# Performance work log

Measured on AMD Instinct MI355X. Metric: run time of the kernel, lower is better.

Reference implementation:

```python
import jax, jax.numpy as jnp
import numpy as np

# SE(3)-equivariant CNN (e3nn/se3cnn-style). The steerable-kernel basis (Clebsch-
# Gordan angular solutions x radial profiles) is a FIXED, non-learned tensor; its
# generating code was not provided, so we use a deterministic random stand-in
# basis of the same shape/contraction structure: kernel = einsum(weights, basis).

K = 7          # conv kernel size
STRIDE = 2
PAD = 3
EPS = 1e-5
BLOCKS = [
    dict(so=8,  vo=4, si=1,  vi=0),
    dict(so=8,  vo=4, si=8,  vi=4),
    dict(so=16, vo=4, si=8,  vi=4),
    dict(so=64, vo=0, si=16, vi=4),
]

def rs_in(b):
    r = [(b['si'], 1)]
    if b['vi'] > 0:
        r += [(b['vi'], 3), (b['vi'], 9)]   # scalars, vectors, 3x3 tensors
    return r

def rs_out(b):
    r = [(b['so'], 1)]
    if b['vo'] > 0:
        r += [(b['vo'], 3)]
    return r

def n_basis(do, di):
    return 3 * min(do, di)   # 3 radial profiles x angular paths (stand-in count)

def _make_bases():
    bases = {}
    for bi, b in enumerate(BLOCKS):
        for oi, (_, do) in enumerate(rs_out(b)):
            for ii, (_, di) in enumerate(rs_in(b)):
                nb = n_basis(do, di)
                rng = np.random.RandomState(1000 * bi + 10 * oi + ii)
                arr = rng.randn(nb, do, di, K, K, K).astype(np.float32)
                bases[(bi, oi, ii)] = jnp.asarray(arr / np.sqrt(nb * di * K ** 3))
    return bases

BASES = _make_bases()

def assemble_kernel(bi, ws):
    b = BLOCKS[bi]
    rows, k = [], 0
    for oi, (mo, do) in enumerate(rs_out(b)):
        cols = []
        for ii, (mi, di) in enumerate(rs_in(b)):
            basis = BASES[(bi, oi, ii)]  # [nb, do, di, K, K, K]
            blk = jnp.einsum('oin,nabxyz->oaibxyz', ws[k], basis)
            cols.append(blk.reshape(mo * do, mi * di, K, K, K))
            k += 1
        rows.append(jnp.concatenate(cols, axis=1))
    return jnp.concatenate(rows, axis=0)  # [C_out, C_in, K, K, K]

def block_forward(bi, x, ws, g_s, g_v, bias):
    b = BLOCKS[bi]
    si, vi, so, vo = b['si'], b['vi'], b['so'], b['vo']
    if vi > 0:  # TensorProduct: outer product of each vector field with itself
        B, _, D, H, W = x.shape
        v = x[:, si:si + 3 * vi].reshape(B, vi, 3, D, H, W)
        t = jnp.einsum('bvixyz,bvjxyz->bvijxyz', v, v).reshape(B, vi * 9, D, H, W)
        x = jnp.concatenate([x, t], axis=1)
    kern = assemble_kernel(bi, ws)
    y = jax.lax.conv_general_dilated(x, kern, (STRIDE,) * 3, [(PAD, PAD)] * 3,
                                     dimension_numbers=('NCDHW', 'OIDHW', 'NCDHW'))
    # SE3BatchNorm (training stats) + BiasRelu (relu on scalars only)
    s = y[:, :so]
    m = s.mean(axis=(0, 2, 3, 4), keepdims=True)
    var = ((s - m) ** 2).mean(axis=(0, 2, 3, 4), keepdims=True)
    s = (s - m) / jnp.sqrt(var + EPS) * g_s[None, :, None, None, None]
    s = jax.nn.relu(s + bias[None, :, None, None, None])
    if vo > 0:
        B2, _, D2, H2, W2 = y.shape
        v = y[:, so:].reshape(B2, vo, 3, D2, H2, W2)
        n2 = (v ** 2).sum(axis=2).mean(axis=(0, 2, 3, 4))  # [vo] mean field norm^2
        v = v / jnp.sqrt(n2 + EPS)[None, :, None, None, None, None]
        v = v * g_v[None, :, None, None, None, None]
        return jnp.concatenate([s, v.reshape(B2, vo * 3, D2, H2, W2)], axis=1)
    return s

def _forward(x, w0_0, w0_1, w1_0, w1_1, w1_2, w1_3, w1_4, w1_5,
             w2_0, w2_1, w2_2, w2_3, w2_4, w2_5, w3_0, w3_1, w3_2,
             g0_s, g0_v, g1_s, g1_v, g2_s, g2_v, g3_s,
             bias0, bias1, bias2, bias3, bn_g, bn_b, lin_w, lin_b):
    ws = [[w0_0, w0_1], [w1_0, w1_1, w1_2, w1_3, w1_4, w1_5],
          [w2_0, w2_1, w2_2, w2_3, w2_4, w2_5], [w3_0, w3_1, w3_2]]
    g_s = [g0_s, g1_s, g2_s, g3_s]
    g_v = [g0_v, g1_v, g2_v, None]
    bias = [bias0, bias1, bias2, bias3]
    # bn_in: BatchNorm3d(1, affine=False), training stats
    m = x.mean(axis=(0, 2, 3, 4), keepdims=True)
    v = ((x - m) ** 2).mean(axis=(0, 2, 3, 4), keepdims=True)
    x = (x - m) / jnp.sqrt(v + EPS)
    for bi in range(4):
        x = block_forward(bi, x, ws[bi], g_s[bi], g_v[bi], bias[bi])
    x = x.mean(axis=(2, 3, 4))  # global spatial mean -> [B, 64]
    mu = x.mean(axis=0, keepdims=True)
    var = ((x - mu) ** 2).mean(axis=0, keepdims=True)
    x = (x - mu) / jnp.sqrt(var + EPS) * bn_g + bn_b
    return x @ lin_w + lin_b

def setup_inputs():
    key = jax.random.key(0)
    ki = [0]
    def nk():
        ki[0] += 1
        return jax.random.fold_in(key, ki[0])
    inp = {'x': jax.random.normal(nk(), (16, 1, 64, 64, 64), dtype=jnp.float32)}
    for bi, b in enumerate(BLOCKS):
        j = 0
        for (mo, do) in rs_out(b):
            for (mi, di) in rs_in(b):
                nb = n_basis(do, di)
                inp[f'w{bi}_{j}'] = 0.2 * jax.random.normal(nk(), (mo, mi, nb), dtype=jnp.float32)
                j += 1
        inp[f'g{bi}_s'] = jnp.ones((b['so'],), jnp.float32)
        if b['vo'] > 0:
            inp[f'g{bi}_v'] = jnp.ones((b['vo'],), jnp.float32)
        inp[f'bias{bi}'] = jnp.zeros((b['so'],), jnp.float32)
    inp['bn_g'] = jnp.ones((64,), jnp.float32)
    inp['bn_b'] = jnp.zeros((64,), jnp.float32)
    inp['lin_w'] = 0.1 * jax.random.normal(nk(), (64, 10), dtype=jnp.float32)
    inp['lin_b'] = jnp.zeros((10,), jnp.float32)
    return inp

def reference(x, w0_0, w0_1, w1_0, w1_1, w1_2, w1_3, w1_4, w1_5,
              w2_0, w2_1, w2_2, w2_3, w2_4, w2_5, w3_0, w3_1, w3_2,
              g0_s, g0_v, g1_s, g1_v, g2_s, g2_v, g3_s,
              bias0, bias1, bias2, bias3, bn_g, bn_b, lin_w, lin_b):
    return _forward(x, w0_0, w0_1, w1_0, w1_1, w1_2, w1_3, w1_4, w1_5,
                    w2_0, w2_1, w2_2, w2_3, w2_4, w2_5, w3_0, w3_1, w3_2,
                    g0_s, g0_v, g1_s, g1_v, g2_s, g2_v, g3_s,
                    bias0, bias1, bias2, bias3, bn_g, bn_b, lin_w, lin_b)
```

## Files before the change

kernel.cpp:

```cpp
#include <hip/hip_runtime.h>
#include <cmath>

constexpr long XN_OFF   = 0;
constexpr long Y0_OFF   = 4194304;
constexpr long Y1_OFF   = 14680064;
constexpr long Y2_OFF   = 15990784;
constexpr long Y3_OFF   = 16220160;
constexpr long K0_OFF   = 16285696;
constexpr long K1_OFF   = 16293536;
constexpr long K2_OFF   = 16732576;
constexpr long K3_OFF   = 17347232;
constexpr long BAS_OFF  = 18952864;
constexpr long SCR_OFF  = 19225552;
constexpr long PARTD_OFF = 20182872;
constexpr long SSD_OFF   = 20191064;
constexpr long ISTD_OFF  = 20191320;
constexpr long POOLD_OFF = 20191324;

struct GenDesc {
  double sdiv[17];
  int seed[17], n[17], scr_off[17], L[17], basis_off[17];
};
struct AsmDesc {
  const float* w[17];
  int cum[18];
  int basis_off[17], row_off[17], col_off[17];
  int dd[17], di[17], mi[17], nb[17], citot[17];
  long koff[17];
};

__global__ __launch_bounds__(256)
void mt_fill_kernel(unsigned int* __restrict__ scratch, GenDesc d) {
  __shared__ unsigned int mt[624];
  const int bb = blockIdx.x;
  const int tid = threadIdx.x;
  if (tid == 0) {
    unsigned int s = (unsigned int)d.seed[bb];
    for (int pos = 0; pos < 624; pos++) {
      mt[pos] = s;
      s = 1812433253u * (s ^ (s >> 30)) + (unsigned)pos + 1u;
    }
  }
  __syncthreads();
  unsigned int* out = scratch + d.scr_off[bb];
  const int L = d.L[bb];
  const int ntw = (L + 623) / 624;
  for (int t = 0; t < ntw; t++) {
    unsigned int v1 = 0, v2 = 0;
    if (tid < 227) { v1 = mt[tid]; v2 = mt[tid + 1]; }
    __syncthreads();
    if (tid < 227) {
      unsigned int y = (v1 & 0x80000000u) | (v2 & 0x7fffffffu);
      mt[tid] = mt[tid + 397] ^ (y >> 1) ^ ((y & 1u) ? 0x9908b0dfu : 0u);
    }
    __syncthreads();
    if (tid < 227) { v1 = mt[227 + tid]; v2 = mt[228 + tid]; }
    __syncthreads();
    if (tid < 227) {
      unsigned int y = (v1 & 0x80000000u) | (v2 & 0x7fffffffu);
      mt[227 + tid] = mt[tid] ^ (y >> 1) ^ ((y & 1u) ? 0x9908b0dfu : 0u);
    }
    __syncthreads();
    if (tid < 170) {
      int i = 454 + tid;
      v1 = mt[i]; v2 = (i < 623) ? mt[i + 1] : mt[0];
    }
    __syncthreads();
    if (tid < 170) {
      int i = 454 + tid;
      unsigned int y = (v1 & 0x80000000u) | (v2 & 0x7fffffffu);
      mt[i] = mt[i - 227] ^ (y >> 1) ^ ((y & 1u) ? 0x9908b0dfu : 0u);
    }
    __syncthreads();
    const int base = t * 624;
    for (int j = tid; j < 624; j += 256) {
      if (base + j < L) {
        unsigned int y = mt[j];
        y ^= y >> 11;
        y ^= (y << 7) & 0x9d2c5680u;
        y ^= (y << 15) & 0xefc60000u;
        y ^= y >> 18;
        out[base + j] = y;
      }
    }
    __syncthreads();
  }
}

__global__ __launch_bounds__(256)
void polar_kernel(const unsigned int* __restrict__ scratch, float* __restrict__ bases, GenDesc d) {
  const int bb = blockIdx.x;
  const int tid = threadIdx.x;
  const int lane = tid & 63, wid = tid >> 6;
  const unsigned int* src = scratch + d.scr_off[bb];
  float* out = bases + d.basis_off[bb];
  const int n = d.n[bb];
  const int P = d.L[bb] >> 2;
  const double sdiv = d.sdiv[bb];
  __shared__ int lds_tot[4];
  int base = 0;
  const int need = (n + 1) >> 1;
  const int nchunk = (P + 255) >> 8;
  for (int ch = 0; ch < nchunk && base < need; ch++) {
    const int p = ch * 256 + tid;
    bool accept = false;
    double x1 = 0.0, x2 = 0.0, r2 = 0.0;
    if (p < P) {
      unsigned int w0 = src[4 * p], w1 = src[4 * p + 1], w2 = src[4 * p + 2], w3 = src[4 * p + 3];
      double u1 = ((double)(w0 >> 5) * 67108864.0 + (double)(w1 >> 6)) * (1.0 / 9007199254740992.0);
      double u2 = ((double)(w2 >> 5) * 67108864.0 + (double)(w3 >> 6)) * (1.0 / 9007199254740992.0);
      x1 = 2.0 * u1 - 1.0; x2 = 2.0 * u2 - 1.0;
      r2 = x1 * x1 + x2 * x2;
      accept = (r2 < 1.0) && (r2 != 0.0);
    }
    unsigned long long mask = __ballot(accept ? 1 : 0);
    int prefix = __popcll(mask & ((1ull << lane) - 1ull));
    int tot = __popcll(mask);
    if (lane == 0) lds_tot[wid] = tot;
    __syncthreads();
    int waveoff = 0;
    #pragma unroll
    for (int w = 0; w < 4; w++) waveoff += (w < wid) ? lds_tot[w] : 0;
    int tot_all = lds_tot[0] + lds_tot[1] + lds_tot[2] + lds_tot[3];
    if (accept) {
      int k = base + waveoff + prefix;
      double f = sqrt(-2.0 * log(r2) / r2);
      int i0 = 2 * k, i1 = 2 * k + 1;
      if (i0 < n) { float g = (float)(f * x2); out[i0] = (float)((double)g / sdiv); }
      if (i1 < n) { float g = (float)(f * x1); out[i1] = (float)((double)g / sdiv); }
    }
    base += tot_all;
    __syncthreads();
  }
}

__global__ void assemble_kernel(const float* __restrict__ bases, float* __restrict__ ws, AsmDesc d) {
  int g = blockIdx.x * 256 + threadIdx.x;
  if (g >= d.cum[17]) return;
  int k = 0;
  while (g >= d.cum[k + 1]) k++;
  int l = g - d.cum[k];
  const int dd = d.dd[k], di = d.di[k], mi = d.mi[k], nb = d.nb[k];
  const int cols = mi * di;
  int tap = l % 343; int rc = l / 343;
  int c = rc % cols; int r = rc / cols;
  int o = r / dd, a = r - o * dd;
  int i = c / di, b2 = c - i * di;
  const float* wp = d.w[k];
  const float* bp = bases + d.basis_off[k] + ((a * di + b2) * 343 + tap);
  const int wbase = (o * mi + i) * nb;
  const int bstride = dd * di * 343;
  double s = 0.0;
  for (int nn = 0; nn < nb; nn++) s += (double)wp[wbase + nn] * (double)bp[(long)nn * bstride];
  int R = d.row_off[k] + r, C = d.col_off[k] + c;
  int t49 = tap / 7, kx = tap - t49 * 7;
  ws[d.koff[k] + ((long)(R * d.citot[k] + C) * 49 + t49) * 8 + kx] = (float)s;
}

template<int CI_TOT, int CO, int ISP, int OSP, int TDX, int TDY, int TDZ,
         int S, int CI_PER, bool ATOMIC, int SI, int CDIR>
__global__ __launch_bounds__(TDX*TDY*TDZ)
void conv3d_kernel(const float* __restrict__ src, const float* __restrict__ kern,
                   float* __restrict__ out) {
  constexpr int NT = TDX * TDY * TDZ;
  constexpr int TILE_X = TDX * S;
  constexpr int IN_X = 2 * TILE_X + 5, IN_Y = 2 * TDY + 5, IN_Z = 2 * TDZ + 5;
  constexpr int IN_XP = IN_X + 1;
  constexpr int IN_TOT = IN_X * IN_Y * IN_Z;
  constexpr int NTX = OSP / TILE_X, NTY = OSP / TDY;
  __shared__ float lds_in[IN_Z * IN_Y * IN_XP + 1];
  const int tid = threadIdx.x;
  const int tx = tid % TDX, ty = (tid / TDX) % TDY, tz = tid / (TDX * TDY);
  const int bx = blockIdx.x;
  const int tXi = bx % NTX, tYi = (bx / NTX) % NTY, tZi = bx / (NTX * NTY);
  const int b = blockIdx.y;
  const int ci0 = blockIdx.z * CI_PER;
  const int gx0 = 2 * (tXi * TILE_X) - 3, gy0 = 2 * (tYi * TDY) - 3, gz0 = 2 * (tZi * TDZ) - 3;

  float acc[S][CO];
  #pragma unroll
  for (int u = 0; u < S; u++)
    #pragma unroll
    for (int c = 0; c < CO; c++) acc[u][c] = 0.f;

  for (int cc = 0; cc < CI_PER; cc++) {
    const int ci = ci0 + cc;
    for (int l = tid; l < IN_TOT; l += NT) {
      int dx = l % IN_X; int t2 = l / IN_X; int dy = t2 % IN_Y; int dz = t2 / IN_Y;
      int gx = gx0 + dx, gy = gy0 + dy, gz = gz0 + dz;
      float v = 0.f;
      if ((unsigned)gx < (unsigned)ISP && (unsigned)gy < (unsigned)ISP &&
          (unsigned)gz < (unsigned)ISP) {
        long spi = ((long)gz * ISP + gy) * ISP + gx;
        if (ci < CDIR) {
          v = src[(long)(b * CDIR + ci) * ISP * ISP * ISP + spi];
        } else {
          int r = ci - CDIR; int vv = r / 9; int ij = r - vv * 9;
          int i2 = ij / 3, j2 = ij - i2 * 3;
          float va = src[(long)(b * CDIR + SI + 3 * vv + i2) * ISP * ISP * ISP + spi];
          float vb = src[(long)(b * CDIR + SI + 3 * vv + j2) * ISP * ISP * ISP + spi];
          v = va * vb;
        }
      }
      int r = dz * IN_Y + dy;
      lds_in[r * IN_XP + dx + ((r >> 1) & 1)] = v;
    }
    __syncthreads();
    float part[S][CO];
    #pragma unroll
    for (int u = 0; u < S; u++)
      #pragma unroll
      for (int c2 = 0; c2 < CO; c2++) part[u][c2] = 0.f;
    for (int kz = 0; kz < 7; kz++) {
      for (int ky = 0; ky < 7; ky++) {
        const int r = (2 * tz + kz) * IN_Y + (2 * ty + ky);
        const int rowbase = r * IN_XP + ((r >> 1) & 1) + 2 * S * tx;
        float strip[2 * S + 5];
        #pragma unroll
        for (int j = 0; j < 2 * S + 5; j++) strip[j] = lds_in[rowbase + j];
        const long wrow0 = (long)ci * 392 + (kz * 7 + ky) * 8;
        #pragma unroll
        for (int c2 = 0; c2 < CO; c2++) {
          const float* __restrict__ wrow = kern + wrow0 + (long)c2 * CI_TOT * 392;
          const float4 wa = *(const float4*)(wrow);
          const float4 wb = *(const float4*)(wrow + 4);
          const float wk[7] = {wa.x, wa.y, wa.z, wa.w, wb.x, wb.y, wb.z};
          #pragma unroll
          for (int kx = 0; kx < 7; kx++) {
            #pragma unroll
            for (int u = 0; u < S; u++)
              part[u][c2] += strip[2 * u + kx] * wk[kx];
          }
        }
      }
    }
    #pragma unroll
    for (int u = 0; u < S; u++)
      #pragma unroll
      for (int c2 = 0; c2 < CO; c2++) acc[u][c2] += part[u][c2];
    __syncthreads();
  }
  const int ozg = tZi * TDZ + tz, oyg = tYi * TDY + ty;
  #pragma unroll
  for (int u = 0; u < S; u++) {
    const int oxg = tXi * TILE_X + tx * S + u;
    #pragma unroll
    for (int co = 0; co < CO; co++) {
      long idx = (((long)(b * CO + co) * OSP + ozg) * OSP + oyg) * OSP + oxg;
      if (ATOMIC) atomicAdd(&out[idx], acc[u][co]);
      else out[idx] = acc[u][co];
    }
  }
}

__global__ __launch_bounds__(256)
void conv_b3_kernel(const float* __restrict__ src, const float* __restrict__ k3,
                    float* __restrict__ out) {
  constexpr int CLS = 580;
  __shared__ float lds_in[16 * CLS];
  const int tid = threadIdx.x;
  const int s = tid & 63, w = tid >> 6;
  const int ox = s & 3, oy = (s >> 2) & 3, oz = s >> 4;
  const int b = blockIdx.y;
  const int cogrp = blockIdx.x >> 2, cch = blockIdx.x & 3;
  const int co0 = cogrp * 16 + w * 4;
  for (int l = tid; l < 16 * 512; l += 256) {
    int cl = l >> 9, sp = l & 511;
    int ci = cch * 16 + cl;
    float v;
    if (ci < 28) v = src[(long)(b * 28 + ci) * 512 + sp];
    else {
      int r = ci - 28; int vv = r / 9; int ij = r - vv * 9;
      int i2 = ij / 3, j2 = ij - i2 * 3;
      v = src[(long)(b * 28 + 16 + 3 * vv + i2) * 512 + sp] *
          src[(long)(b * 28 + 16 + 3 * vv + j2) * 512 + sp];
    }
    int r = sp >> 3;
    lds_in[cl * CLS + r * 9 + (sp & 7) + ((r >> 1) & 1)] = v;
  }
  __syncthreads();
  float acc[4] = {0.f, 0.f, 0.f, 0.f};
  for (int cl = 0; cl < 16; cl++) {
    const int ci = cch * 16 + cl;
    float part[4] = {0.f, 0.f, 0.f, 0.f};
    for (int kz = 0; kz < 7; kz++) {
      const int iz = 2 * oz + kz - 3;
      const bool vz = (unsigned)iz < 8u;
      for (int ky = 0; ky < 7; ky++) {
        const int iy = 2 * oy + ky - 3;
        const bool vyz = vz && ((unsigned)iy < 8u);
        const int r = iz * 8 + iy;
        const int rowbase = cl * CLS + r * 9 + ((r >> 1) & 1);
        float strip[7];
        #pragma unroll
        for (int kx = 0; kx < 7; kx++) {
          const int ix = 2 * ox + kx - 3;
          strip[kx] = (vyz && (unsigned)ix < 8u) ? lds_in[rowbase + ix] : 0.f;
        }
        #pragma unroll
        for (int j = 0; j < 4; j++) {
          const float* __restrict__ wr =
              k3 + ((long)((co0 + j) * 64 + ci) * 49 + (kz * 7 + ky)) * 8;
          const float4 wa = *(const float4*)(wr);
          const float4 wb = *(const float4*)(wr + 4);
          const float wk[7] = {wa.x, wa.y, wa.z, wa.w, wb.x, wb.y, wb.z};
          #pragma unroll
          for (int kx = 0; kx < 7; kx++) part[j] += strip[kx] * wk[kx];
        }
      }
    }
    #pragma unroll
    for (int j = 0; j < 4; j++) acc[j] += part[j];
  }
  #pragma unroll
  for (int j = 0; j < 4; j++)
    atomicAdd(&out[(long)(b * 64 + co0 + j) * 64 + s], acc[j]);
}

__device__ inline void block_reduce2d(double& s, double& q) {
  #pragma unroll
  for (int o = 32; o > 0; o >>= 1) { s += __shfl_down(s, o); q += __shfl_down(q, o); }
  __shared__ double ls[8];
  const int lane = threadIdx.x & 63, wid = threadIdx.x >> 6;
  if (lane == 0) { ls[wid * 2] = s; ls[wid * 2 + 1] = q; }
  __syncthreads();
  if (threadIdx.x == 0) {
    for (int w = 1; w < 4; w++) { s += ls[w * 2]; q += ls[w * 2 + 1]; }
  }
}

__global__ __launch_bounds__(256)
void in_part_kernel(const float* __restrict__ x, double* __restrict__ part) {
  double s = 0.0, q = 0.0;
  const long base = (long)blockIdx.x * 4096;
  for (int i = threadIdx.x; i < 4096; i += 256) {
    double v = (double)x[base + i]; s += v; q += v * v;
  }
  block_reduce2d(s, q);
  if (threadIdx.x == 0) { part[blockIdx.x * 2] = s; part[blockIdx.x * 2 + 1] = q; }
}

__global__ __launch_bounds__(256)
void in_final_kernel(const double* __restrict__ part, double* __restrict__ st) {
  double s = 0.0, q = 0.0;
  for (int i = threadIdx.x; i < 1024; i += 256) { s += part[i * 2]; q += part[i * 2 + 1]; }
  block_reduce2d(s, q);
  if (threadIdx.x == 0) {
    const double invN = 1.0 / 4194304.0;
    double m = s * invN;
    double var = q * invN - m * m;
    st[0] = m; st[1] = 1.0 / sqrt(var + 1e-5);
  }
}

__global__ void in_apply_kernel(const float* __restrict__ x, const double* __restrict__ st,
                                float* __restrict__ xn) {
  long i = (long)blockIdx.x * 256 + threadIdx.x;
  if (i < 4194304) xn[i] = (float)(((double)x[i] - st[0]) * st[1]);
}

__global__ __launch_bounds__(256)
void stats_partial_kernel(const float* __restrict__ y, double* __restrict__ part,
                          int C, int SP, int P) {
  const int c = blockIdx.x / P, p = blockIdx.x % P;
  const int chunk = SP / P;
  double s = 0.0, q = 0.0;
  for (int b = 0; b < 16; b++) {
    const float* base = y + (long)(b * C + c) * SP + (long)p * chunk;
    for (int i = threadIdx.x; i < chunk; i += 256) {
      double v = (double)base[i]; s += v; q += v * v;
    }
  }
  block_reduce2d(s, q);
  if (threadIdx.x == 0) { part[blockIdx.x * 2] = s; part[blockIdx.x * 2 + 1] = q; }
}

__global__ __launch_bounds__(256)
void stats_final_kernel(const double* __restrict__ part, double* __restrict__ ss,
                        const float* __restrict__ g_s, const float* __restrict__ g_v,
                        const float* __restrict__ bias, int C, int P, int so, double invcount) {
  __shared__ double lsq[64];
  const int c = threadIdx.x;
  double s = 0.0, q = 0.0;
  if (c < C) {
    for (int p = 0; p < P; p++) { s += part[(c * P + p) * 2]; q += part[(c * P + p) * 2 + 1]; }
    lsq[c] = q;
  }
  __syncthreads();
  if (c < C) {
    if (c < so) {
      double m = s * invcount;
      double var = q * invcount - m * m;
      double rstd = 1.0 / sqrt(var + 1e-5);
      double sc = (double)g_s[c] * rstd;
      ss[c * 2] = sc; ss[c * 2 + 1] = (double)bias[c] - m * sc;
    } else {
      int v = (c - so) / 3;
      double n2 = (lsq[so + 3 * v] + lsq[so + 3 * v + 1] + lsq[so + 3 * v + 2]) * invcount;
      ss[c * 2] = (double)g_v[v] / sqrt(n2 + 1e-5);
      ss[c * 2 + 1] = 0.0;
    }
  }
}

__global__ void apply_kernel(float* __restrict__ y, const double* __restrict__ ss,
                             int C, int SP, int so, long total) {
  long idx = (long)blockIdx.x * 256 + threadIdx.x;
  if (idx >= total) return;
  int c = (int)((idx / SP) % C);
  double v = (double)y[idx] * ss[c * 2] + ss[c * 2 + 1];
  if (c < so) v = fmax(v, 0.0);
  y[idx] = (float)v;
}

__global__ void pool_kernel(const float* __restrict__ y3, double* __restrict__ pooled) {
  int t = blockIdx.x * 256 + threadIdx.x;
  if (t < 1024) {
    double s = 0.0;
    for (int i = 0; i < 64; i++) s += (double)y3[(long)t * 64 + i];
    pooled[t] = s * (1.0 / 64.0);
  }
}

__global__ __launch_bounds__(256)
void head_kernel(const double* __restrict__ pooled, const float* __restrict__ bn_g,
                 const float* __restrict__ bn_b, const float* __restrict__ lin_w,
                 const float* __restrict__ lin_b, float* __restrict__ out) {
  __shared__ double p[1024];
  for (int i = threadIdx.x; i < 1024; i += 256) p[i] = pooled[i];
  __syncthreads();
  if (threadIdx.x < 64) {
    int c = threadIdx.x;
    double s = 0.0, q = 0.0;
    for (int b = 0; b < 16; b++) { double v = p[b * 64 + c]; s += v; q += v * v; }
    double m = s * (1.0 / 16.0);
    double var = q * (1.0 / 16.0) - m * m;
    double rstd = 1.0 / sqrt(var + 1e-5);
    for (int b = 0; b < 16; b++)
      p[b * 64 + c] = (p[b * 64 + c] - m) * rstd * (double)bn_g[c] + (double)bn_b[c];
  }
  __syncthreads();
  if (threadIdx.x < 160) {
    int b = threadIdx.x / 10, j = threadIdx.x - b * 10;
    double s = (double)lin_b[j];
    for (int c = 0; c < 64; c++) s += p[b * 64 + c] * (double)lin_w[c * 10 + j];
    out[b * 10 + j] = (float)s;
  }
}

extern "C" void kernel_launch(void* const* d_in, const int* in_sizes, int n_in,
                              void* d_out, int out_size, void* d_ws, size_t ws_size,
                              hipStream_t stream) {
  (void)in_sizes; (void)n_in; (void)out_size; (void)ws_size;
  float* W = (float*)d_ws;
  double* PARTD = (double*)(W + PARTD_OFF);
  double* SSD   = (double*)(W + SSD_OFF);
  double* ISTD  = (double*)(W + ISTD_OFF);
  double* POOLD = (double*)(W + POOLD_OFF);

  static const int k_bi[17]  = {0,0, 1,1,1,1,1,1, 2,2,2,2,2,2, 3,3,3};
  static const int k_oi[17]  = {0,1, 0,0,0,1,1,1, 0,0,0,1,1,1, 0,0,0};
  static const int k_ii[17]  = {0,0, 0,1,2,0,1,2, 0,1,2,0,1,2, 0,1,2};
  static const int k_do[17]  = {1,3, 1,1,1,3,3,3, 1,1,1,3,3,3, 1,1,1};
  static const int k_dI[17]  = {1,1, 1,3,9,1,3,9, 1,3,9,1,3,9, 1,3,9};
  static const int k_mo[17]  = {8,4, 8,8,8,4,4,4, 16,16,16,4,4,4, 64,64,64};
  static const int k_mi[17]  = {1,1, 8,4,4,8,4,4, 8,4,4,8,4,4, 16,4,4};
  static const int k_row[17] = {0,8, 0,0,0,8,8,8, 0,0,0,16,16,16, 0,0,0};
  static const int k_col[17] = {0,0, 0,8,20,0,8,20, 0,8,20,0,8,20, 0,16,28};
  static const int k_win[17] = {1,2, 6,7,8,9,10,11, 15,16,17,18,19,20, 24,25,26};
  static const int citot_by_bi[4] = {1, 56, 56, 64};
  static const long koff_by_bi[4] = {K0_OFF, K1_OFF, K2_OFF, K3_OFF};

  GenDesc gd;
  AsmDesc ad;
  int scr = 0, boff = 0, cum = 0;
  ad.cum[0] = 0;
  for (int k = 0; k < 17; k++) {
    int bi = k_bi[k];
    int dd = k_do[k], di = k_dI[k];
    int nb = 3 * (dd < di ? dd : di);
    int n = nb * dd * di * 343;
    gd.seed[k] = 1000 * bi + 10 * k_oi[k] + k_ii[k];
    gd.n[k] = n;
    int P = (3 * n) / 4 + 2048;
    gd.L[k] = 4 * P;
    gd.scr_off[k] = scr; scr += gd.L[k];
    gd.basis_off[k] = boff; boff += n;
    gd.sdiv[k] = sqrt((double)(nb * di * 343));
    ad.w[k] = (const float*)d_in[k_win[k]];
    ad.basis_off[k] = gd.basis_off[k];
    ad.row_off[k] = k_row[k]; ad.col_off[k] = k_col[k];
    ad.dd[k] = dd; ad.di[k] = di; ad.mi[k] = k_mi[k]; ad.nb[k] = nb;
    ad.citot[k] = citot_by_bi[bi];
    ad.koff[k] = koff_by_bi[bi];
    cum += k_mo[k] * dd * k_mi[k] * di * 343;
    ad.cum[k + 1] = cum;
  }

  const float* x     = (const float*)d_in[0];
  const float* g0_s  = (const float*)d_in[3];
  const float* g0_v  = (const float*)d_in[4];
  const float* bias0 = (const float*)d_in[5];
  const float* g1_s  = (const float*)d_in[12];
  const float* g1_v  = (const float*)d_in[13];
  const float* bias1 = (const float*)d_in[14];
  const float* g2_s  = (const float*)d_in[21];
  const float* g2_v  = (const float*)d_in[22];
  const float* bias2 = (const float*)d_in[23];
  const float* g3_s  = (const float*)d_in[27];
  const float* bias3 = (const float*)d_in[28];
  const float* bn_g  = (const float*)d_in[29];
  const float* bn_b  = (const float*)d_in[30];
  const float* lin_w = (const float*)d_in[31];
  const float* lin_b = (const float*)d_in[32];

  hipMemsetAsync(W + Y1_OFF, 0, 1310720 * 4, stream);
  hipMemsetAsync(W + Y2_OFF, 0, 229376 * 4, stream);
  hipMemsetAsync(W + Y3_OFF, 0, 65536 * 4, stream);

  mt_fill_kernel<<<17, 256, 0, stream>>>((unsigned int*)(W + SCR_OFF), gd);
  polar_kernel<<<17, 256, 0, stream>>>((const unsigned int*)(W + SCR_OFF), W + BAS_OFF, gd);
  assemble_kernel<<<(cum + 255) / 256, 256, 0, stream>>>(W + BAS_OFF, W, ad);

  in_part_kernel<<<1024, 256, 0, stream>>>(x, PARTD);
  in_final_kernel<<<1, 256, 0, stream>>>(PARTD, ISTD);
  in_apply_kernel<<<16384, 256, 0, stream>>>(x, ISTD, W + XN_OFF);

  conv3d_kernel<1, 20, 64, 32, 4, 8, 8, 2, 1, false, 0, 1>
      <<<dim3(64, 16, 1), 256, 0, stream>>>(W + XN_OFF, W + K0_OFF, W + Y0_OFF);
  stats_partial_kernel<<<20 * 32, 256, 0, stream>>>(W + Y0_OFF, PARTD, 20, 32768, 32);
  stats_final_kernel<<<1, 256, 0, stream>>>(PARTD, SSD, g0_s, g0_v, bias0,
                                            20, 32, 8, 1.0 / 524288.0);
  apply_kernel<<<40960, 256, 0, stream>>>(W + Y0_OFF, SSD, 20, 32768, 8, 10485760L);

  conv3d_kernel<56, 20, 32, 16, 4, 8, 8, 2, 7, true, 8, 20>
      <<<dim3(8, 16, 8), 256, 0, stream>>>(W + Y0_OFF, W + K1_OFF, W + Y1_OFF);
  stats_partial_kernel<<<20 * 8, 256, 0, stream>>>(W + Y1_OFF, PARTD, 20, 4096, 8);
  stats_final_kernel<<<1, 256, 0, stream>>>(PARTD, SSD, g1_s, g1_v, bias1,
                                            20, 8, 8, 1.0 / 65536.0);
  apply_kernel<<<5120, 256, 0, stream>>>(W + Y1_OFF, SSD, 20, 4096, 8, 1310720L);

  conv3d_kernel<56, 28, 16, 8, 4, 8, 4, 1, 4, true, 8, 20>
      <<<dim3(4, 16, 14), 128, 0, stream>>>(W + Y1_OFF, W + K2_OFF, W + Y2_OFF);
  stats_partial_kernel<<<28 * 2, 256, 0, stream>>>(W + Y2_OFF, PARTD, 28, 512, 2);
  stats_final_kernel<<<1, 256, 0, stream>>>(PARTD, SSD, g2_s, g2_v, bias2,
                                            28, 2, 16, 1.0 / 8192.0);
  apply_kernel<<<896, 256, 0, stream>>>(W + Y2_OFF, SSD, 28, 512, 16, 229376L);

  conv_b3_kernel<<<dim3(16, 16), 256, 0, stream>>>(W + Y2_OFF, W + K3_OFF, W + Y3_OFF);
  stats_partial_kernel<<<64, 256, 0, stream>>>(W + Y3_OFF, PARTD, 64, 64, 1);
  stats_final_kernel<<<1, 256, 0, stream>>>(PARTD, SSD, g3_s, nullptr, bias3,
                                            64, 1, 64, 1.0 / 1024.0);
  apply_kernel<<<256, 256, 0, stream>>>(W + Y3_OFF, SSD, 64, 64, 64, 65536L);

  pool_kernel<<<4, 256, 0, stream>>>(W + Y3_OFF, POOLD);
  head_kernel<<<1, 256, 0, stream>>>(POOLD, bn_g, bn_b, lin_w, lin_b, (float*)d_out);
}
```

Measured before the change: 2.311 ms.

## Parallelize polar Box-Muller rejection sampling via count-scan-write passes

The single-block-per-basis polar rejection sampler is split into three kernels: a per-group acceptance count over 16 groups per basis, a small prefix scan over the group counts, and a write pass where each group starts from its scanned base offset. This spreads the serial rejection loop across many more blocks, at the cost of two extra launches and evaluating each candidate twice. The block-2 convolution template is also retuned to a different tile parameter, which halves its grid in x.

```diff
diff --git a/kernel.cpp b/kernel.cpp
--- a/kernel.cpp
+++ b/kernel.cpp
@@ -16,6 +16,11 @@
 constexpr long SSD_OFF   = 20191064;
 constexpr long ISTD_OFF  = 20191320;
 constexpr long POOLD_OFF = 20191324;
+constexpr long CNT_OFF   = 20193372;
+constexpr long GBASE_OFF = 20193644;
+
+constexpr int PGRP = 4096;
+constexpr int MAXG = 16;
 
 struct GenDesc {
   double sdiv[17];
@@ -87,32 +92,73 @@
   }
 }
 
-__global__ __launch_bounds__(256)
-void polar_kernel(const unsigned int* __restrict__ scratch, float* __restrict__ bases, GenDesc d) {
-  const int bb = blockIdx.x;
+__device__ inline bool polar_accept(const unsigned int* src, int p,
+                                    double& x1, double& x2, double& r2) {
+  unsigned int w0 = src[4 * p], w1 = src[4 * p + 1], w2 = src[4 * p + 2], w3 = src[4 * p + 3];
+  double u1 = ((double)(w0 >> 5) * 67108864.0 + (double)(w1 >> 6)) * (1.0 / 9007199254740992.0);
+  double u2 = ((double)(w2 >> 5) * 67108864.0 + (double)(w3 >> 6)) * (1.0 / 9007199254740992.0);
+  x1 = 2.0 * u1 - 1.0; x2 = 2.0 * u2 - 1.0;
+  r2 = x1 * x1 + x2 * x2;
+  return (r2 < 1.0) && (r2 != 0.0);
+}
+
+__global__ __launch_bounds__(256)
+void polar_count_kernel(const unsigned int* __restrict__ scratch, int* __restrict__ counts,
+                        GenDesc d) {
+  const int bb = blockIdx.y, grp = blockIdx.x, tid = threadIdx.x;
+  const unsigned int* src = scratch + d.scr_off[bb];
+  const int P = d.L[bb] >> 2;
+  const int p0 = grp * PGRP;
+  int cnt = 0;
+  if (p0 < P) {
+    const int p1 = min(p0 + PGRP, P);
+    for (int p = p0 + tid; p < p1; p += 256) {
+      double x1, x2, r2;
+      if (polar_accept(src, p, x1, x2, r2)) cnt++;
+    }
+  }
+  #pragma unroll
+  for (int o = 32; o > 0; o >>= 1) cnt += __shfl_down(cnt, o);
+  __shared__ int ws4[4];
+  if ((tid & 63) == 0) ws4[tid >> 6] = cnt;
+  __syncthreads();
+  if (tid == 0) counts[bb * MAXG + grp] = ws4[0] + ws4[1] + ws4[2] + ws4[3];
+}
+
+__global__ void polar_scan_kernel(const int* __restrict__ counts, int* __restrict__ gbase) {
+  int bb = threadIdx.x;
+  if (bb < 17) {
+    int acc = 0;
+    for (int g = 0; g < MAXG; g++) {
+      gbase[bb * MAXG + g] = acc;
+      acc += counts[bb * MAXG + g];
+    }
+  }
+}
+
+__global__ __launch_bounds__(256)
+void polar_write_kernel(const unsigned int* __restrict__ scratch, const int* __restrict__ gbase,
+                        float* __restrict__ bases, GenDesc d) {
+  const int bb = blockIdx.y, grp = blockIdx.x;
   const int tid = threadIdx.x;
   const int lane = tid & 63, wid = tid >> 6;
   const unsigned int* src = scratch + d.scr_off[bb];
   float* out = bases + d.basis_off[bb];
   const int n = d.n[bb];
+  const int need = (n + 1) >> 1;
   const int P = d.L[bb] >> 2;
+  const int p0 = grp * PGRP;
+  if (p0 >= P) return;
+  int base = gbase[bb * MAXG + grp];
+  if (base >= need) return;
   const double sdiv = d.sdiv[bb];
+  const int p1 = min(p0 + PGRP, P);
   __shared__ int lds_tot[4];
-  int base = 0;
-  const int need = (n + 1) >> 1;
-  const int nchunk = (P + 255) >> 8;
-  for (int ch = 0; ch < nchunk && base < need; ch++) {
-    const int p = ch * 256 + tid;
+  for (int ch = p0; ch < p1 && base < need; ch += 256) {
+    const int p = ch + tid;
     bool accept = false;
     double x1 = 0.0, x2 = 0.0, r2 = 0.0;
-    if (p < P) {
-      unsigned int w0 = src[4 * p], w1 = src[4 * p + 1], w2 = src[4 * p + 2], w3 = src[4 * p + 3];
-      double u1 = ((double)(w0 >> 5) * 67108864.0 + (double)(w1 >> 6)) * (1.0 / 9007199254740992.0);
-      double u2 = ((double)(w2 >> 5) * 67108864.0 + (double)(w3 >> 6)) * (1.0 / 9007199254740992.0);
-      x1 = 2.0 * u1 - 1.0; x2 = 2.0 * u2 - 1.0;
-      r2 = x1 * x1 + x2 * x2;
-      accept = (r2 < 1.0) && (r2 != 0.0);
-    }
+    if (p < p1) accept = polar_accept(src, p, x1, x2, r2);
     unsigned long long mask = __ballot(accept ? 1 : 0);
     int prefix = __popcll(mask & ((1ull << lane) - 1ull));
     int tot = __popcll(mask);
@@ -457,6 +503,8 @@
   double* SSD   = (double*)(W + SSD_OFF);
   double* ISTD  = (double*)(W + ISTD_OFF);
   double* POOLD = (double*)(W + POOLD_OFF);
+  int* CNT   = (int*)(W + CNT_OFF);
+  int* GBASE = (int*)(W + GBASE_OFF);
 
   static const int k_bi[17]  = {0,0, 1,1,1,1,1,1, 2,2,2,2,2,2, 3,3,3};
   static const int k_oi[17]  = {0,1, 0,0,0,1,1,1, 0,0,0,1,1,1, 0,0,0};
@@ -519,7 +567,11 @@
   hipMemsetAsync(W + Y3_OFF, 0, 65536 * 4, stream);
 
   mt_fill_kernel<<<17, 256, 0, stream>>>((unsigned int*)(W + SCR_OFF), gd);
-  polar_kernel<<<17, 256, 0, stream>>>((const unsigned int*)(W + SCR_OFF), W + BAS_OFF, gd);
+  polar_count_kernel<<<dim3(MAXG, 17), 256, 0, stream>>>((const unsigned int*)(W + SCR_OFF),
+                                                         CNT, gd);
+  polar_scan_kernel<<<1, 32, 0, stream>>>(CNT, GBASE);
+  polar_write_kernel<<<dim3(MAXG, 17), 256, 0, stream>>>((const unsigned int*)(W + SCR_OFF),
+                                                         GBASE, W + BAS_OFF, gd);
   assemble_kernel<<<(cum + 255) / 256, 256, 0, stream>>>(W + BAS_OFF, W, ad);
 
   in_part_kernel<<<1024, 256, 0, stream>>>(x, PARTD);
@@ -540,8 +592,8 @@
                                             20, 8, 8, 1.0 / 65536.0);
   apply_kernel<<<5120, 256, 0, stream>>>(W + Y1_OFF, SSD, 20, 4096, 8, 1310720L);
 
-  conv3d_kernel<56, 28, 16, 8, 4, 8, 4, 1, 4, true, 8, 20>
-      <<<dim3(4, 16, 14), 128, 0, stream>>>(W + Y1_OFF, W + K2_OFF, W + Y2_OFF);
+  conv3d_kernel<56, 28, 16, 8, 4, 8, 4, 2, 4, true, 8, 20>
+      <<<dim3(2, 16, 14), 128, 0, stream>>>(W + Y1_OFF, W + K2_OFF, W + Y2_OFF);
   stats_partial_kernel<<<28 * 2, 256, 0, stream>>>(W + Y2_OFF, PARTD, 28, 512, 2);
   stats_final_kernel<<<1, 256, 0, stream>>>(PARTD, SSD, g2_s, g2_v, bias2,
                                             28, 2, 16, 1.0 / 8192.0);
```

Result: faster. 2.144 ms (-7.2%).
